# Kernel optimization log

Measured on AMD Instinct MI355X. Metric: run time of the kernel, lower is better.

The kernel has to match this reference:

```python
import jax, jax.numpy as jnp
from jax import lax
import numpy as np

B, C, H, W = 32, 3, 224, 224
NUM_CLASSES = 100
K = 3  # kernel size
OUT1 = 32


def _bn(x, g, b, m, v, eps=1e-5):
    # eval-mode batchnorm over channel dim of NCHW
    inv = g / jnp.sqrt(v + eps)
    return x * inv[None, :, None, None] + (b - m * inv)[None, :, None, None]


def _conv(x, w, pad=1):
    return lax.conv_general_dilated(
        x, w, (1, 1), ((pad, pad), (pad, pad)),
        dimension_numbers=('NCHW', 'OIHW', 'NCHW'))


def _maxpool2(x):
    return lax.reduce_window(x, -jnp.inf, lax.max, (1, 1, 2, 2), (1, 1, 2, 2), 'VALID')


def setup_inputs() -> dict:
    key = jax.random.key(0)
    ks = jax.random.split(key, 32)
    n = lambda k, s, sc=0.05: jax.random.normal(k, s, jnp.float32) * sc
    u = lambda k, s: jax.random.uniform(k, s, jnp.float32, 0.5, 1.5)
    inp = {
        'x': jax.random.normal(ks[0], (B, C, H, W), jnp.float32),
        # weight_gen MLP: Linear(3,128)->ReLU->Linear(128,256)->ReLU->Linear(256, 32*3*3*3)
        'w1': n(ks[1], (128, C)), 'b1': n(ks[2], (128,)),
        'w2': n(ks[3], (256, 128)), 'b2': n(ks[4], (256,)),
        'w3': n(ks[5], (OUT1 * C * K * K, 256)), 'b3': n(ks[6], (OUT1 * C * K * K,)),
        # bias_gen: Linear(3, 32)
        'wb': n(ks[7], (OUT1, C)), 'bb': n(ks[8], (OUT1,)),
        'conv2_w': n(ks[9], (64, 32, 3, 3)), 'conv2_b': n(ks[10], (64,)),
        'conv3_w': n(ks[11], (128, 64, 3, 3)), 'conv3_b': n(ks[12], (128,)),
        'bn1_g': 1.0 + n(ks[13], (32,)), 'bn1_b': n(ks[14], (32,)), 'bn1_m': n(ks[15], (32,)), 'bn1_v': u(ks[16], (32,)),
        'bn2_g': 1.0 + n(ks[17], (64,)), 'bn2_b': n(ks[18], (64,)), 'bn2_m': n(ks[19], (64,)), 'bn2_v': u(ks[20], (64,)),
        'bn3_g': 1.0 + n(ks[21], (128,)), 'bn3_b': n(ks[22], (128,)), 'bn3_m': n(ks[23], (128,)), 'bn3_v': u(ks[24], (128,)),
        'fc_w': n(ks[25], (NUM_CLASSES, 128)), 'fc_b': n(ks[26], (NUM_CLASSES,)),
    }
    return inp


def reference(x, w1, b1, w2, b2, w3, b3, wb, bb, conv2_w, conv2_b, conv3_w, conv3_b,
              bn1_g, bn1_b, bn1_m, bn1_v, bn2_g, bn2_b, bn2_m, bn2_v,
              bn3_g, bn3_b, bn3_m, bn3_v, fc_w, fc_b):
    Bx = x.shape[0]
    # DynamicConv2D: channel indicator is all-ones since C == max_in_channels
    ind = jnp.ones((Bx, C), x.dtype)
    h = jax.nn.relu(ind @ w1.T + b1)
    h = jax.nn.relu(h @ w2.T + b2)
    dyn_w = (h @ w3.T + b3).reshape(Bx, OUT1, C, K, K)  # per-sample [O,I,k,k]
    dyn_b = ind @ wb.T + bb                             # per-sample [O]
    # vmap over batch: one single-image conv per sample with its own weights
    y = jax.vmap(lambda xi, wi, bi: _conv(xi[None], wi)[0] + bi[:, None, None])(x, dyn_w, dyn_b)
    y = jax.nn.relu(_bn(y, bn1_g, bn1_b, bn1_m, bn1_v))
    y = _maxpool2(y)
    y = jax.nn.relu(_bn(_conv(y, conv2_w) + conv2_b[None, :, None, None], bn2_g, bn2_b, bn2_m, bn2_v))
    y = _maxpool2(y)
    y = jax.nn.relu(_bn(_conv(y, conv3_w) + conv3_b[None, :, None, None], bn3_g, bn3_b, bn3_m, bn3_v))
    y = y.mean(axis=(2, 3))  # AdaptiveAvgPool2d((1,1)) + flatten
    # dropout is identity in eval
    return y @ fc_w.T + fc_b
```

## Files before the change

kernel.cpp:

```cpp
#include <hip/hip_runtime.h>
#include <hip/hip_bf16.h>

#define BATCH 32
#define HW1 224

typedef __attribute__((ext_vector_type(8))) short short8;
typedef __attribute__((ext_vector_type(4))) float floatx4;

static __device__ __forceinline__ unsigned short f2bf(float f) {
    unsigned int u = __float_as_uint(f);
    unsigned int r = (u + 0x7fffu + ((u >> 16) & 1u)) >> 16;
    return (unsigned short)r;
}

typedef __attribute__((address_space(1))) const unsigned int guint;
typedef __attribute__((address_space(3))) unsigned int suint;
static __device__ __forceinline__ void gload_lds16(const void* g, void* l) {
    __builtin_amdgcn_global_load_lds((guint*)g, (suint*)l, 16, 0, 0);
}

#define MFMA(A, B, C) __builtin_amdgcn_mfma_f32_16x16x32_bf16((A), (B), (C), 0, 0, 0)

__global__ __launch_bounds__(256) void gen_dynw_repack(
    const float* __restrict__ w1, const float* __restrict__ b1,
    const float* __restrict__ w2, const float* __restrict__ b2,
    const float* __restrict__ w3, const float* __restrict__ b3,
    const float* __restrict__ conv2_w, const float* __restrict__ conv3_w,
    const float* __restrict__ wb, const float* __restrict__ bb,
    const float* __restrict__ conv2_b, const float* __restrict__ conv3_b,
    const float* __restrict__ bn1_g, const float* __restrict__ bn1_b,
    const float* __restrict__ bn1_m, const float* __restrict__ bn1_v,
    const float* __restrict__ bn2_g, const float* __restrict__ bn2_b,
    const float* __restrict__ bn2_m, const float* __restrict__ bn2_v,
    const float* __restrict__ bn3_g, const float* __restrict__ bn3_b,
    const float* __restrict__ bn3_m, const float* __restrict__ bn3_v,
    float* __restrict__ dwt,
    unsigned short* __restrict__ wrep2, unsigned short* __restrict__ wrep3,
    float* __restrict__ bn1_s, float* __restrict__ bn1_t,
    float* __restrict__ bn2_s, float* __restrict__ bn2_t,
    float* __restrict__ bn3_s, float* __restrict__ bn3_t,
    float* __restrict__ feat)
{
    __shared__ float h1s[128];
    __shared__ float h2s[256];
    const int blk = blockIdx.x;
    const int t = threadIdx.x;
    if (blk < 216) {
        if (t < 128) {
            float s = b1[t] + w1[t*3+0] + w1[t*3+1] + w1[t*3+2];
            h1s[t] = fmaxf(s, 0.f);
        }
        __syncthreads();
        {
            float s0 = b2[t], s1 = 0.f, s2 = 0.f, s3 = 0.f;
            const float* wr = w2 + (size_t)t*128;
#pragma unroll 4
            for (int k = 0; k < 128; k += 4) {
                float4 wv = *(const float4*)(wr + k);
                s0 = fmaf(wv.x, h1s[k  ], s0);
                s1 = fmaf(wv.y, h1s[k+1], s1);
                s2 = fmaf(wv.z, h1s[k+2], s2);
                s3 = fmaf(wv.w, h1s[k+3], s3);
            }
            h2s[t] = fmaxf((s0 + s1) + (s2 + s3), 0.f);
        }
        __syncthreads();
        const int wave = t >> 6, lane = t & 63;
        const int row = blk*4 + wave;
        float4 wv = *(const float4*)(w3 + (size_t)row*256 + lane*4);
        float4 hv = *(const float4*)&h2s[lane*4];
        float s = wv.x*hv.x + wv.y*hv.y + wv.z*hv.z + wv.w*hv.w;
#pragma unroll
        for (int m = 1; m < 64; m <<= 1) s += __shfl_xor(s, m);
        if (lane == 0) {
            int oc = row / 27, tap = row - oc*27;
            dwt[tap*32 + oc] = s + b3[row];
        }
    } else if (blk < 576) {
        const int i = (blk - 216)*256 + t;
        const int N2 = 9*64*32;
        if (i < N2) {
            int tp = i / (64*32); int rem = i - tp*(64*32);
            int oc = rem >> 5, ic = rem & 31;
            wrep2[i] = f2bf(conv2_w[(oc*32 + ic)*9 + tp]);
        } else {
            int j = i - N2;
            int tp = j / (128*64); int rem = j - tp*(128*64);
            int oc = rem >> 6, ic = rem & 63;
            wrep3[j] = f2bf(conv3_w[(oc*64 + ic)*9 + tp]);
        }
    } else {
        if (t < 32) {
            float dynb = bb[t] + wb[t*3+0] + wb[t*3+1] + wb[t*3+2];
            float s = bn1_g[t] / sqrtf(bn1_v[t] + 1e-5f);
            bn1_s[t] = s;
            bn1_t[t] = (dynb - bn1_m[t]) * s + bn1_b[t];
        }
        if (t < 64) {
            float s = bn2_g[t] / sqrtf(bn2_v[t] + 1e-5f);
            bn2_s[t] = s;
            bn2_t[t] = (conv2_b[t] - bn2_m[t]) * s + bn2_b[t];
        }
        if (t < 128) {
            float s = bn3_g[t] / sqrtf(bn3_v[t] + 1e-5f);
            bn3_s[t] = s;
            bn3_t[t] = (conv3_b[t] - bn3_m[t]) * s + bn3_b[t];
        }
        for (int i = t; i < BATCH*128; i += 256) feat[i] = 0.f;
    }
}

__global__ __launch_bounds__(256) void conv1_pool(
    const float* __restrict__ x, const float* __restrict__ dwt,
    const float* __restrict__ bn_s, const float* __restrict__ bn_t,
    unsigned short* __restrict__ act1)
{
    __shared__ __align__(16) unsigned short sp[18*18*4];
    __shared__ __align__(16) unsigned short swA[32*32];
    __shared__ __align__(16) unsigned short swB[32*32];

    const int tid = threadIdx.x;
    const int bx = blockIdx.x, by = blockIdx.y, b = blockIdx.z;
    const int gx0 = bx*16 - 1, gy0 = by*16 - 1;
    const float* xb = x + (size_t)b * 3 * HW1 * HW1;

    for (int i = tid; i < 1024; i += 256) { swA[i] = 0; swB[i] = 0; }

    float v[2][3];
#pragma unroll
    for (int k = 0; k < 2; ++k) {
        int i = tid + k*256;
        v[k][0] = 0.f; v[k][1] = 0.f; v[k][2] = 0.f;
        if (i < 324) {
            int r = i / 18, c = i - r*18;
            int gy = gy0 + r, gx = gx0 + c;
            if ((unsigned)gy < HW1 && (unsigned)gx < HW1) {
                const float* pp = xb + gy*HW1 + gx;
                v[k][0] = pp[0];
                v[k][1] = pp[HW1*HW1];
                v[k][2] = pp[2*HW1*HW1];
            }
        }
    }
#pragma unroll
    for (int k = 0; k < 2; ++k) {
        int i = tid + k*256;
        if (i < 324) {
            unsigned int lo = (unsigned int)f2bf(v[k][0]) |
                              ((unsigned int)f2bf(v[k][1]) << 16);
            unsigned int hi = (unsigned int)f2bf(v[k][2]);
            *(uint2*)&sp[i*4] = make_uint2(lo, hi);
        }
    }
    __syncthreads();

#pragma unroll
    for (int k = 0; k < 4; ++k) {
        int i = tid + k*256;
        if (i < 864) {
            int tap = i >> 5, oc = i & 31;
            int ic = tap / 9, kk = tap - ic*9;
            int ky = kk / 3, kx = kk - ky*3;
            unsigned short w = f2bf(dwt[i]);
            if (kk == 8)      swB[oc*32 + ic] = w;
            else if (kx < 2)  swA[oc*32 + ky*8 + kx*4 + ic] = w;
            else              swA[oc*32 + 3*8  + ky*4 + ic] = w;
        }
    }
    __syncthreads();

    const int lane = tid & 63, wave = tid >> 6;
    const int n = lane & 15, quad = lane >> 4;

    short8 afrA[2], afrB[2];
#pragma unroll
    for (int h = 0; h < 2; ++h) {
        afrA[h] = *(const short8*)&swA[((h*16 + n)*32) + quad*8];
        afrB[h] = *(const short8*)&swB[((h*16 + n)*32) + quad*8];
    }
    float4 sv[2], tv[2];
#pragma unroll
    for (int h = 0; h < 2; ++h) {
        sv[h] = *(const float4*)(bn_s + h*16 + quad*4);
        tv[h] = *(const float4*)(bn_t + h*16 + quad*4);
    }

    union U { short8 s8; uint2 u2[2]; };

    const int y0w = wave*4;
    float ev[2][4];

#pragma unroll
    for (int yi = 0; yi < 4; ++yi) {
        const int y = y0w + yi;
        int r0 = (quad < 3) ? (y + quad) : y;
        int c0 = (quad < 3) ? n : (n + 2);
        int r1 = (quad < 3) ? (y + quad) : (y + 1);
        int c1 = (quad < 3) ? (n + 1) : (n + 2);
        U bf1;
        bf1.u2[0] = *(const uint2*)&sp[(r0*18 + c0)*4];
        bf1.u2[1] = *(const uint2*)&sp[(r1*18 + c1)*4];
        U bf2;
        bf2.u2[0] = *(const uint2*)&sp[((y+2)*18 + (n+2))*4];
        bf2.u2[1] = bf2.u2[0];

        float vr[2][4];
#pragma unroll
        for (int h = 0; h < 2; ++h) {
            floatx4 acc = {0.f, 0.f, 0.f, 0.f};
            acc = MFMA(afrA[h], bf1.s8, acc);
            acc = MFMA(afrB[h], bf2.s8, acc);
            float sj[4] = {sv[h].x, sv[h].y, sv[h].z, sv[h].w};
            float tj[4] = {tv[h].x, tv[h].y, tv[h].z, tv[h].w};
#pragma unroll
            for (int j = 0; j < 4; ++j)
                vr[h][j] = fmaxf(fmaf(acc[j], sj[j], tj[j]), 0.f);
        }

        if ((yi & 1) == 0) {
#pragma unroll
            for (int h = 0; h < 2; ++h)
#pragma unroll
                for (int j = 0; j < 4; ++j) ev[h][j] = vr[h][j];
        } else {
            int py = by*8 + ((y0w + yi) >> 1);
            int px = bx*8 + (n >> 1);
            unsigned short* dstp =
                act1 + ((size_t)((b*112 + py)*112 + px))*32 + quad*4;
#pragma unroll
            for (int h = 0; h < 2; ++h) {
                unsigned int pk[2];
#pragma unroll
                for (int j = 0; j < 4; ++j) {
                    float m = fmaxf(vr[h][j], ev[h][j]);
                    m = fmaxf(m, __shfl_xor(m, 1));
                    unsigned short us = f2bf(m);
                    if (j & 1) pk[j >> 1] |= ((unsigned int)us) << 16;
                    else       pk[j >> 1]  = us;
                }
                if (!(n & 1)) *(uint2*)(dstp + h*16) = *(uint2*)pk;
            }
        }
    }
}

__global__ __launch_bounds__(256) void conv2_mfma(
    const unsigned short* __restrict__ act1,
    const unsigned short* __restrict__ wrep,
    const float* __restrict__ bn_s, const float* __restrict__ bn_t,
    unsigned short* __restrict__ act2)
{
    constexpr int IC = 32, OC = 64, H = 112;
    __shared__ __align__(16) short lds[4*18*18*8];

    const int tid = threadIdx.x;
    const int b = blockIdx.z;
    const int cx0 = blockIdx.x*16, cy0 = blockIdx.y*16;
    const unsigned short* ab = act1 + (size_t)b*H*H*IC;

    unsigned bad = 0;
    {
        int k = 0;
        for (int s = tid; s < 4*324; s += 256, ++k) {
            int ck = s / 324; int rem = s - ck*324;
            int y = rem / 18, xx = rem - y*18;
            int gy = cy0 - 1 + y, gx = cx0 - 1 + xx;
            if (!(((unsigned)gy < H) && ((unsigned)gx < H))) {
                bad |= 1u << k; gy = 0; gx = 0;
            }
            gload_lds16(ab + (size_t)(gy*H + gx)*IC + ck*8, &lds[s*8]);
        }
        if (bad) {
            asm volatile("s_waitcnt vmcnt(0)" ::: "memory");
            k = 0;
            for (int s = tid; s < 4*324; s += 256, ++k)
                if (bad & (1u << k)) {
                    uint4 z = {0u,0u,0u,0u};
                    *(uint4*)&lds[s*8] = z;
                }
        }
    }

    const int lane = tid & 63, wave = tid >> 6;
    const int n = lane & 15, quad = lane >> 4;
    const int oc0w = wave * 16;

    short8 afr[9];
#pragma unroll
    for (int t = 0; t < 9; ++t)
        afr[t] = *(const short8*)(wrep + (size_t)(t*OC + oc0w + n)*IC + quad*8);

    float4 sv = *(const float4*)(bn_s + oc0w + quad*4);
    float4 tv = *(const float4*)(bn_t + oc0w + quad*4);
    float sj[4] = {sv.x, sv.y, sv.z, sv.w};
    float tj[4] = {tv.x, tv.y, tv.z, tv.w};

    __syncthreads();

    floatx4 acc[3];
    float ev[4];

#pragma unroll
    for (int r = 0; r < 18; ++r) {
        const short* rp = &lds[((quad*18 + r)*18 + n)*8];
        short8 w0 = *(const short8*)(rp);
        short8 w1 = *(const short8*)(rp + 8);
        short8 w2 = *(const short8*)(rp + 16);

        if (r < 16) {
            floatx4 a = {0.f,0.f,0.f,0.f};
            a = MFMA(afr[0], w0, a);
            a = MFMA(afr[1], w1, a);
            a = MFMA(afr[2], w2, a);
            acc[r % 3] = a;
        }
        if (r >= 1 && r <= 16) {
            int y = r - 1;
            floatx4 a = acc[y % 3];
            a = MFMA(afr[3], w0, a);
            a = MFMA(afr[4], w1, a);
            a = MFMA(afr[5], w2, a);
            acc[y % 3] = a;
        }
        if (r >= 2) {
            int y = r - 2;
            floatx4 a = acc[y % 3];
            a = MFMA(afr[6], w0, a);
            a = MFMA(afr[7], w1, a);
            a = MFMA(afr[8], w2, a);

            float v[4];
#pragma unroll
            for (int j = 0; j < 4; ++j)
                v[j] = fmaxf(fmaf(a[j], sj[j], tj[j]), 0.f);

            if ((y & 1) == 0) {
#pragma unroll
                for (int j = 0; j < 4; ++j) ev[j] = v[j];
            } else {
                unsigned int pk[2];
#pragma unroll
                for (int j = 0; j < 4; ++j) {
                    float m = fmaxf(v[j], ev[j]);
                    m = fmaxf(m, __shfl_xor(m, 1));
                    unsigned short us = f2bf(m);
                    if (j & 1) pk[j >> 1] |= ((unsigned int)us) << 16;
                    else       pk[j >> 1]  = us;
                }
                if (!(n & 1)) {
                    int py = (cy0 >> 1) + (y >> 1), px = (cx0 >> 1) + (n >> 1);
                    unsigned short* dstp =
                        act2 + ((size_t)((b*56 + py)*56 + px))*OC + oc0w + quad*4;
                    *(uint2*)dstp = *(uint2*)pk;
                }
            }
        }
    }
}

__global__ __launch_bounds__(256) void conv3_mfma(
    const unsigned short* __restrict__ act2,
    const unsigned short* __restrict__ wrep,
    const float* __restrict__ bn_s, const float* __restrict__ bn_t,
    float* __restrict__ feat)
{
    constexpr int IC = 64, OC = 128, H = 56;
    __shared__ __align__(16) short lds[8*9*18*8];

    const int tid = threadIdx.x;
    const int b = blockIdx.z >> 1, half = blockIdx.z & 1;
    const int cx0 = blockIdx.x*16, cy0 = blockIdx.y*7;
    const unsigned short* ab = act2 + (size_t)b*H*H*IC;

    unsigned bad = 0;
    {
        int k = 0;
        for (int s = tid; s < 8*9*18; s += 256, ++k) {
            int ck = s / (9*18); int rem = s - ck*(9*18);
            int y = rem / 18, xx = rem - y*18;
            int gy = cy0 - 1 + y, gx = cx0 - 1 + xx;
            if (!(((unsigned)gy < H) && ((unsigned)gx < H))) {
                bad |= 1u << k; gy = 0; gx = 0;
            }
            gload_lds16(ab + (size_t)(gy*H + gx)*IC + ck*8, &lds[s*8]);
        }
        if (bad) {
            asm volatile("s_waitcnt vmcnt(0)" ::: "memory");
            k = 0;
            for (int s = tid; s < 8*9*18; s += 256, ++k)
                if (bad & (1u << k)) {
                    uint4 z = {0u,0u,0u,0u};
                    *(uint4*)&lds[s*8] = z;
                }
        }
    }

    const int lane = tid & 63, wave = tid >> 6;
    const int n = lane & 15, quad = lane >> 4;
    const int oc0w = half*64 + wave*16;

    short8 afr[18];
#pragma unroll
    for (int t = 0; t < 9; ++t)
#pragma unroll
        for (int kc = 0; kc < 2; ++kc)
            afr[t*2 + kc] = *(const short8*)(wrep + (size_t)(t*OC + oc0w + n)*IC + kc*32 + quad*8);

    float4 sv = *(const float4*)(bn_s + oc0w + quad*4);
    float4 tv = *(const float4*)(bn_t + oc0w + quad*4);
    float sj[4] = {sv.x, sv.y, sv.z, sv.w};
    float tj[4] = {tv.x, tv.y, tv.z, tv.w};

    __syncthreads();

    float sum[4] = {0.f, 0.f, 0.f, 0.f};
    const bool vx = (cx0 + n) < H;
    floatx4 acc[3];

#pragma unroll
    for (int r = 0; r < 9; ++r) {
        const short* p0 = &lds[((quad*9     + r)*18 + n)*8];
        const short* p1 = &lds[(((4+quad)*9 + r)*18 + n)*8];
        short8 a0 = *(const short8*)(p0);
        short8 a1 = *(const short8*)(p0 + 8);
        short8 a2 = *(const short8*)(p0 + 16);
        short8 b0 = *(const short8*)(p1);
        short8 b1 = *(const short8*)(p1 + 8);
        short8 b2 = *(const short8*)(p1 + 16);

        if (r < 7) {
            floatx4 a = {0.f,0.f,0.f,0.f};
            a = MFMA(afr[0], a0, a);
            a = MFMA(afr[1], b0, a);
            a = MFMA(afr[2], a1, a);
            a = MFMA(afr[3], b1, a);
            a = MFMA(afr[4], a2, a);
            a = MFMA(afr[5], b2, a);
            acc[r % 3] = a;
        }
        if (r >= 1 && r <= 7) {
            int y = r - 1;
            floatx4 a = acc[y % 3];
            a = MFMA(afr[6],  a0, a);
            a = MFMA(afr[7],  b0, a);
            a = MFMA(afr[8],  a1, a);
            a = MFMA(afr[9],  b1, a);
            a = MFMA(afr[10], a2, a);
            a = MFMA(afr[11], b2, a);
            acc[y % 3] = a;
        }
        if (r >= 2) {
            int y = r - 2;
            floatx4 a = acc[y % 3];
            a = MFMA(afr[12], a0, a);
            a = MFMA(afr[13], b0, a);
            a = MFMA(afr[14], a1, a);
            a = MFMA(afr[15], b1, a);
            a = MFMA(afr[16], a2, a);
            a = MFMA(afr[17], b2, a);
            if (vx) {
#pragma unroll
                for (int j = 0; j < 4; ++j)
                    sum[j] += fmaxf(fmaf(a[j], sj[j], tj[j]), 0.f);
            }
        }
    }
#pragma unroll
    for (int j = 0; j < 4; ++j) {
        sum[j] += __shfl_xor(sum[j], 1);
        sum[j] += __shfl_xor(sum[j], 2);
        sum[j] += __shfl_xor(sum[j], 4);
        sum[j] += __shfl_xor(sum[j], 8);
    }
    if (n == 0) {
#pragma unroll
        for (int j = 0; j < 4; ++j)
            atomicAdd(&feat[b*128 + oc0w + quad*4 + j], sum[j]);
    }
}

__global__ __launch_bounds__(256) void fc_kernel(
    const float* __restrict__ feat, const float* __restrict__ fc_w,
    const float* __restrict__ fc_b, float* __restrict__ out)
{
    int g = blockIdx.x * 16 + (threadIdx.x >> 4);
    int l = threadIdx.x & 15;
    if (g >= BATCH*100) return;
    int b = g / 100, n = g - b*100;
    const float* f = feat + b*128 + l*8;
    const float* w = fc_w + (size_t)n*128 + l*8;
    float4 f0 = *(const float4*)(f);
    float4 f1 = *(const float4*)(f + 4);
    float4 w0 = *(const float4*)(w);
    float4 w1 = *(const float4*)(w + 4);
    float s = f0.x*w0.x + f0.y*w0.y + f0.z*w0.z + f0.w*w0.w
            + f1.x*w1.x + f1.y*w1.y + f1.z*w1.z + f1.w*w1.w;
    s += __shfl_xor(s, 1);
    s += __shfl_xor(s, 2);
    s += __shfl_xor(s, 4);
    s += __shfl_xor(s, 8);
    if (l == 0) out[g] = s * (1.f/3136.f) + fc_b[n];
}

extern "C" void kernel_launch(void* const* d_in, const int* in_sizes, int n_in,
                              void* d_out, int out_size, void* d_ws, size_t ws_size,
                              hipStream_t stream)
{
    const float* x       = (const float*)d_in[0];
    const float* w1      = (const float*)d_in[1];
    const float* b1      = (const float*)d_in[2];
    const float* w2      = (const float*)d_in[3];
    const float* b2      = (const float*)d_in[4];
    const float* w3      = (const float*)d_in[5];
    const float* b3      = (const float*)d_in[6];
    const float* wb      = (const float*)d_in[7];
    const float* bb      = (const float*)d_in[8];
    const float* conv2_w = (const float*)d_in[9];
    const float* conv2_b = (const float*)d_in[10];
    const float* conv3_w = (const float*)d_in[11];
    const float* conv3_b = (const float*)d_in[12];
    const float* bn1_g = (const float*)d_in[13];
    const float* bn1_b = (const float*)d_in[14];
    const float* bn1_m = (const float*)d_in[15];
    const float* bn1_v = (const float*)d_in[16];
    const float* bn2_g = (const float*)d_in[17];
    const float* bn2_b = (const float*)d_in[18];
    const float* bn2_m = (const float*)d_in[19];
    const float* bn2_v = (const float*)d_in[20];
    const float* bn3_g = (const float*)d_in[21];
    const float* bn3_b = (const float*)d_in[22];
    const float* bn3_m = (const float*)d_in[23];
    const float* bn3_v = (const float*)d_in[24];
    const float* fc_w  = (const float*)d_in[25];
    const float* fc_b  = (const float*)d_in[26];
    float* out = (float*)d_out;

    char* wsb = (char*)d_ws;
    float* ws    = (float*)d_ws;
    float* dwt   = ws;
    float* bn1_s = ws + 864;
    float* bn1_t = ws + 896;
    float* bn2_s = ws + 928;
    float* bn2_t = ws + 992;
    float* bn3_s = ws + 1056;
    float* bn3_t = ws + 1184;
    float* feat  = ws + 1312;
    unsigned short* wrep2 = (unsigned short*)(wsb + 32768);
    unsigned short* wrep3 = (unsigned short*)(wsb + 69632);
    unsigned short* act1  = (unsigned short*)(wsb + 262144);
    unsigned short* act2  = (unsigned short*)(wsb + 262144 + 25690112);

    gen_dynw_repack<<<577, 256, 0, stream>>>(
        w1, b1, w2, b2, w3, b3, conv2_w, conv3_w,
        wb, bb, conv2_b, conv3_b,
        bn1_g, bn1_b, bn1_m, bn1_v, bn2_g, bn2_b, bn2_m, bn2_v,
        bn3_g, bn3_b, bn3_m, bn3_v,
        dwt, wrep2, wrep3,
        bn1_s, bn1_t, bn2_s, bn2_t, bn3_s, bn3_t, feat);

    conv1_pool<<<dim3(14, 14, BATCH), 256, 0, stream>>>(
        x, dwt, bn1_s, bn1_t, act1);

    conv2_mfma<<<dim3(7, 7, BATCH), 256, 0, stream>>>(
        act1, wrep2, bn2_s, bn2_t, act2);

    conv3_mfma<<<dim3(4, 8, BATCH*2), 256, 0, stream>>>(
        act2, wrep3, bn3_s, bn3_t, feat);

    fc_kernel<<<200, 256, 0, stream>>>(feat, fc_w, fc_b, out);
}
```

Measured before the change: 190.5 us.

## Prepack conv1 bf16 weights upstream, vectorize input loads, enlarge conv3 row tile

The weight generator now writes the dynamic conv1 weights as bf16, already placed in the MFMA fragment layout, to a workspace buffer. Each conv1 block then copies that buffer into LDS with one 16-byte load per thread plus masking, instead of converting 864 floats and zeroing two LDS arrays itself. Conv1 also reads the input as float2 pairs into a padded 20-wide LDS tile, so fewer threads issue fewer, wider loads. Conv3 now covers 14 output rows per block instead of 7, which halves the grid and cuts halo reloads, at the cost of more LDS per block and fewer blocks to spread across the GPU.

```diff
diff --git a/kernel.cpp b/kernel.cpp
--- a/kernel.cpp
+++ b/kernel.cpp
@@ -34,7 +34,7 @@
     const float* __restrict__ bn2_m, const float* __restrict__ bn2_v,
     const float* __restrict__ bn3_g, const float* __restrict__ bn3_b,
     const float* __restrict__ bn3_m, const float* __restrict__ bn3_v,
-    float* __restrict__ dwt,
+    unsigned short* __restrict__ swpre,
     unsigned short* __restrict__ wrep2, unsigned short* __restrict__ wrep3,
     float* __restrict__ bn1_s, float* __restrict__ bn1_t,
     float* __restrict__ bn2_s, float* __restrict__ bn2_t,
@@ -74,7 +74,14 @@
         for (int m = 1; m < 64; m <<= 1) s += __shfl_xor(s, m);
         if (lane == 0) {
             int oc = row / 27, tap = row - oc*27;
-            dwt[tap*32 + oc] = s + b3[row];
+            int ic = tap / 9, kk = tap - ic*9;
+            int ky = kk / 3, kx = kk - ky*3;
+            unsigned short v = f2bf(s + b3[row]);
+            int pos;
+            if (kk == 8)      pos = 1024 + oc*32 + ic;
+            else if (kx < 2)  pos = oc*32 + ky*8 + kx*4 + ic;
+            else              pos = oc*32 + 24 + ky*4 + ic;
+            swpre[pos] = v;
         }
     } else if (blk < 576) {
         const int i = (blk - 216)*256 + t;
@@ -111,61 +118,48 @@
 }
 
 __global__ __launch_bounds__(256) void conv1_pool(
-    const float* __restrict__ x, const float* __restrict__ dwt,
+    const float* __restrict__ x,
+    const unsigned short* __restrict__ swpre,
     const float* __restrict__ bn_s, const float* __restrict__ bn_t,
     unsigned short* __restrict__ act1)
 {
-    __shared__ __align__(16) unsigned short sp[18*18*4];
-    __shared__ __align__(16) unsigned short swA[32*32];
-    __shared__ __align__(16) unsigned short swB[32*32];
+    __shared__ __align__(16) unsigned short sp[18*20*4];
+    __shared__ __align__(16) unsigned short swAB[2048];
 
     const int tid = threadIdx.x;
     const int bx = blockIdx.x, by = blockIdx.y, b = blockIdx.z;
-    const int gx0 = bx*16 - 1, gy0 = by*16 - 1;
+    const int gy0 = by*16 - 1;
+    const int gxs0 = bx*16 - 2;
     const float* xb = x + (size_t)b * 3 * HW1 * HW1;
 
-    for (int i = tid; i < 1024; i += 256) { swA[i] = 0; swB[i] = 0; }
-
-    float v[2][3];
-#pragma unroll
-    for (int k = 0; k < 2; ++k) {
-        int i = tid + k*256;
-        v[k][0] = 0.f; v[k][1] = 0.f; v[k][2] = 0.f;
-        if (i < 324) {
-            int r = i / 18, c = i - r*18;
-            int gy = gy0 + r, gx = gx0 + c;
-            if ((unsigned)gy < HW1 && (unsigned)gx < HW1) {
-                const float* pp = xb + gy*HW1 + gx;
-                v[k][0] = pp[0];
-                v[k][1] = pp[HW1*HW1];
-                v[k][2] = pp[2*HW1*HW1];
-            }
-        }
-    }
-#pragma unroll
-    for (int k = 0; k < 2; ++k) {
-        int i = tid + k*256;
-        if (i < 324) {
-            unsigned int lo = (unsigned int)f2bf(v[k][0]) |
-                              ((unsigned int)f2bf(v[k][1]) << 16);
-            unsigned int hi = (unsigned int)f2bf(v[k][2]);
-            *(uint2*)&sp[i*4] = make_uint2(lo, hi);
-        }
-    }
-    __syncthreads();
-
-#pragma unroll
-    for (int k = 0; k < 4; ++k) {
-        int i = tid + k*256;
-        if (i < 864) {
-            int tap = i >> 5, oc = i & 31;
-            int ic = tap / 9, kk = tap - ic*9;
-            int ky = kk / 3, kx = kk - ky*3;
-            unsigned short w = f2bf(dwt[i]);
-            if (kk == 8)      swB[oc*32 + ic] = w;
-            else if (kx < 2)  swA[oc*32 + ky*8 + kx*4 + ic] = w;
-            else              swA[oc*32 + 3*8  + ky*4 + ic] = w;
-        }
+    {
+        uint4 w = *(const uint4*)(swpre + tid*8);
+        if (tid < 128) {
+            w.y &= 0xFFFFu; w.w &= 0xFFFFu;
+        } else if (((tid*8) & 31) != 0) {
+            w.x = 0u; w.y = 0u; w.z = 0u; w.w = 0u;
+        } else {
+            w.y &= 0xFFFFu; w.z = 0u; w.w = 0u;
+        }
+        *(uint4*)&swAB[tid*8] = w;
+    }
+
+    float2 c0 = {0.f, 0.f}, c1 = {0.f, 0.f}, c2 = {0.f, 0.f};
+    if (tid < 180) {
+        int row = tid / 10, p = tid - row*10;
+        int gy = gy0 + row, gx = gxs0 + p*2;
+        if (((unsigned)gy < HW1) && ((unsigned)gx <= 222u)) {
+            const float* pp = xb + gy*HW1 + gx;
+            c0 = *(const float2*)(pp);
+            c1 = *(const float2*)(pp + HW1*HW1);
+            c2 = *(const float2*)(pp + 2*HW1*HW1);
+        }
+        uint4 v;
+        v.x = (unsigned int)f2bf(c0.x) | ((unsigned int)f2bf(c1.x) << 16);
+        v.y = (unsigned int)f2bf(c2.x);
+        v.z = (unsigned int)f2bf(c0.y) | ((unsigned int)f2bf(c1.y) << 16);
+        v.w = (unsigned int)f2bf(c2.y);
+        *(uint4*)&sp[tid*8] = v;
     }
     __syncthreads();
 
@@ -175,8 +169,8 @@
     short8 afrA[2], afrB[2];
 #pragma unroll
     for (int h = 0; h < 2; ++h) {
-        afrA[h] = *(const short8*)&swA[((h*16 + n)*32) + quad*8];
-        afrB[h] = *(const short8*)&swB[((h*16 + n)*32) + quad*8];
+        afrA[h] = *(const short8*)&swAB[((h*16 + n)*32) + quad*8];
+        afrB[h] = *(const short8*)&swAB[1024 + ((h*16 + n)*32) + quad*8];
     }
     float4 sv[2], tv[2];
 #pragma unroll
@@ -194,14 +188,14 @@
     for (int yi = 0; yi < 4; ++yi) {
         const int y = y0w + yi;
         int r0 = (quad < 3) ? (y + quad) : y;
-        int c0 = (quad < 3) ? n : (n + 2);
+        int c0i = (quad < 3) ? n : (n + 2);
         int r1 = (quad < 3) ? (y + quad) : (y + 1);
-        int c1 = (quad < 3) ? (n + 1) : (n + 2);
+        int c1i = (quad < 3) ? (n + 1) : (n + 2);
         U bf1;
-        bf1.u2[0] = *(const uint2*)&sp[(r0*18 + c0)*4];
-        bf1.u2[1] = *(const uint2*)&sp[(r1*18 + c1)*4];
+        bf1.u2[0] = *(const uint2*)&sp[(r0*20 + c0i + 1)*4];
+        bf1.u2[1] = *(const uint2*)&sp[(r1*20 + c1i + 1)*4];
         U bf2;
-        bf2.u2[0] = *(const uint2*)&sp[((y+2)*18 + (n+2))*4];
+        bf2.u2[0] = *(const uint2*)&sp[((y+2)*20 + (n+3))*4];
         bf2.u2[1] = bf2.u2[0];
 
         float vr[2][4];
@@ -365,18 +359,18 @@
     float* __restrict__ feat)
 {
     constexpr int IC = 64, OC = 128, H = 56;
-    __shared__ __align__(16) short lds[8*9*18*8];
+    __shared__ __align__(16) short lds[8*16*18*8];
 
     const int tid = threadIdx.x;
     const int b = blockIdx.z >> 1, half = blockIdx.z & 1;
-    const int cx0 = blockIdx.x*16, cy0 = blockIdx.y*7;
+    const int cx0 = blockIdx.x*16, cy0 = blockIdx.y*14;
     const unsigned short* ab = act2 + (size_t)b*H*H*IC;
 
     unsigned bad = 0;
     {
         int k = 0;
-        for (int s = tid; s < 8*9*18; s += 256, ++k) {
-            int ck = s / (9*18); int rem = s - ck*(9*18);
+        for (int s = tid; s < 8*16*18; s += 256, ++k) {
+            int ck = s / (16*18); int rem = s - ck*(16*18);
             int y = rem / 18, xx = rem - y*18;
             int gy = cy0 - 1 + y, gx = cx0 - 1 + xx;
             if (!(((unsigned)gy < H) && ((unsigned)gx < H))) {
@@ -387,7 +381,7 @@
         if (bad) {
             asm volatile("s_waitcnt vmcnt(0)" ::: "memory");
             k = 0;
-            for (int s = tid; s < 8*9*18; s += 256, ++k)
+            for (int s = tid; s < 8*16*18; s += 256, ++k)
                 if (bad & (1u << k)) {
                     uint4 z = {0u,0u,0u,0u};
                     *(uint4*)&lds[s*8] = z;
@@ -418,9 +412,9 @@
     floatx4 acc[3];
 
 #pragma unroll
-    for (int r = 0; r < 9; ++r) {
-        const short* p0 = &lds[((quad*9     + r)*18 + n)*8];
-        const short* p1 = &lds[(((4+quad)*9 + r)*18 + n)*8];
+    for (int r = 0; r < 16; ++r) {
+        const short* p0 = &lds[((quad*16     + r)*18 + n)*8];
+        const short* p1 = &lds[(((4+quad)*16 + r)*18 + n)*8];
         short8 a0 = *(const short8*)(p0);
         short8 a1 = *(const short8*)(p0 + 8);
         short8 a2 = *(const short8*)(p0 + 16);
@@ -428,7 +422,7 @@
         short8 b1 = *(const short8*)(p1 + 8);
         short8 b2 = *(const short8*)(p1 + 16);
 
-        if (r < 7) {
+        if (r < 14) {
             floatx4 a = {0.f,0.f,0.f,0.f};
             a = MFMA(afr[0], a0, a);
             a = MFMA(afr[1], b0, a);
@@ -438,7 +432,7 @@
             a = MFMA(afr[5], b2, a);
             acc[r % 3] = a;
         }
-        if (r >= 1 && r <= 7) {
+        if (r >= 1 && r <= 14) {
             int y = r - 1;
             floatx4 a = acc[y % 3];
             a = MFMA(afr[6],  a0, a);
@@ -537,7 +531,6 @@
 
     char* wsb = (char*)d_ws;
     float* ws    = (float*)d_ws;
-    float* dwt   = ws;
     float* bn1_s = ws + 864;
     float* bn1_t = ws + 896;
     float* bn2_s = ws + 928;
@@ -545,6 +538,7 @@
     float* bn3_s = ws + 1056;
     float* bn3_t = ws + 1184;
     float* feat  = ws + 1312;
+    unsigned short* swpre = (unsigned short*)(wsb + 24576);
     unsigned short* wrep2 = (unsigned short*)(wsb + 32768);
     unsigned short* wrep3 = (unsigned short*)(wsb + 69632);
     unsigned short* act1  = (unsigned short*)(wsb + 262144);
@@ -555,16 +549,16 @@
         wb, bb, conv2_b, conv3_b,
         bn1_g, bn1_b, bn1_m, bn1_v, bn2_g, bn2_b, bn2_m, bn2_v,
         bn3_g, bn3_b, bn3_m, bn3_v,
-        dwt, wrep2, wrep3,
+        swpre, wrep2, wrep3,
         bn1_s, bn1_t, bn2_s, bn2_t, bn3_s, bn3_t, feat);
 
     conv1_pool<<<dim3(14, 14, BATCH), 256, 0, stream>>>(
-        x, dwt, bn1_s, bn1_t, act1);
+        x, swpre, bn1_s, bn1_t, act1);
 
     conv2_mfma<<<dim3(7, 7, BATCH), 256, 0, stream>>>(
         act1, wrep2, bn2_s, bn2_t, act2);
 
-    conv3_mfma<<<dim3(4, 8, BATCH*2), 256, 0, stream>>>(
+    conv3_mfma<<<dim3(4, 4, BATCH*2), 256, 0, stream>>>(
         act2, wrep3, bn3_s, bn3_t, feat);
 
     fc_kernel<<<200, 256, 0, stream>>>(feat, fc_w, fc_b, out);
```

Result: faster. 181.2 us (-4.9%).
